# Kernel optimization log

Hardware: AMD Instinct MI355X
Metric: run time of the kernel (lower is better)

The kernel has to match this reference:

```python
import jax, jax.numpy as jnp
import numpy as np

IMAGE_SIZE = 512
OUT_SIZE = 64
FEAT = 256
SCALES = [2.0, 4.0, 6.0]
RATIOS = [0.5, 1.0, 2.0]
POS_THR = 0.7
NEG_THR = 0.3
HW = OUT_SIZE - 2            # head grid after 3x3 VALID conv
A = len(SCALES) * len(RATIOS)
B, N = 16, 8


def _anchor_base():
    # mirrors get_anchor_base(out_size-2, ratios, scales): w=scale*ratio, h=scale,
    # centers at i+0.5, boxes [xmin,ymin,xmax,ymax] clipped to [0, HW]
    ctr = np.arange(HW, dtype=np.float32) + 0.5
    ws = np.array([s * r for r in RATIOS for s in SCALES], np.float32)
    hs = np.array([s for r in RATIOS for s in SCALES], np.float32)
    X = ctr[:, None, None]  # x index first, as in the torch loop
    Y = ctr[None, :, None]
    xmin = np.clip(X - ws / 2, 0, HW)
    xmax = np.clip(X + ws / 2, 0, HW)
    ymin = np.clip(Y - hs / 2, 0, HW)
    ymax = np.clip(Y + hs / 2, 0, HW)
    xmin, ymin, xmax, ymax = np.broadcast_arrays(xmin, ymin, xmax, ymax)
    return np.stack([xmin, ymin, xmax, ymax], -1).reshape(-1, 4)  # [T,4]


def _conv(x, w, b):
    y = jax.lax.conv_general_dilated(x, w, (1, 1), 'VALID',
                                     dimension_numbers=('NCHW', 'OIHW', 'NCHW'))
    return y + b[None, :, None, None]


def setup_inputs() -> dict:
    key = jax.random.key(0)
    ks = jax.random.split(key, 8)
    features = jax.random.normal(ks[0], (B, FEAT, OUT_SIZE, OUT_SIZE), jnp.float32)
    cxy = jax.random.uniform(ks[1], (B, N, 2), jnp.float32, 0.0, IMAGE_SIZE)
    half = jax.random.uniform(ks[2], (B, N, 2), jnp.float32, 10.0, 60.0)
    mins = jnp.clip(cxy - half, 0.0, IMAGE_SIZE)
    maxs = jnp.clip(cxy + half, 0.0, IMAGE_SIZE)
    gt_boxes = jnp.concatenate([mins, maxs], -1)  # [B,N,4] xyxy in image coords
    gt_class = jax.random.randint(ks[3], (B, N), 0, 21)
    conv_w = jax.random.normal(ks[4], (FEAT, FEAT, 3, 3), jnp.float32) * 0.02
    conv_b = jnp.zeros((FEAT,), jnp.float32)
    cls_w = jax.random.normal(ks[5], (A, FEAT, 1, 1), jnp.float32) * 0.02
    cls_b = jnp.zeros((A,), jnp.float32)
    box_w = jax.random.normal(ks[6], (4 * A, FEAT, 1, 1), jnp.float32) * 0.02
    box_b = jnp.zeros((4 * A,), jnp.float32)
    return dict(features=features, gt_boxes=gt_boxes, gt_class=gt_class,
                conv_w=conv_w, conv_b=conv_b, cls_w=cls_w, cls_b=cls_b,
                box_w=box_w, box_b=box_b)


def reference(features, gt_boxes, gt_class, conv_w, conv_b, cls_w, cls_b, box_w, box_b):
    b = features.shape[0]
    x = _conv(features, conv_w, conv_b)          # [B,FEAT,HW,HW]
    cls = _conv(x, cls_w, cls_b)                 # [B,A,HW,HW]
    bx = _conv(x, box_w, box_b)                  # [B,4A,HW,HW]
    cls = cls.transpose(0, 2, 3, 1).reshape(b, -1)                    # [B,T]
    pred_off = bx.transpose(0, 2, 3, 1).reshape(b, -1, 4)             # [B,T,4]

    anchors = jnp.asarray(_anchor_base())        # [T,4]
    scale = IMAGE_SIZE // HW
    gt = gt_boxes / scale                        # project_bboxes p2a

    ax1, ay1, ax2, ay2 = (anchors[:, i] for i in range(4))
    gx1, gy1, gx2, gy2 = (gt[..., i] for i in range(4))
    area_a = (ax2 - ax1) * (ay2 - ay1)                                 # [T]
    area_g = (gx2 - gx1) * (gy2 - gy1)                                 # [B,N]
    ix1 = jnp.maximum(ax1[None, :, None], gx1[:, None, :])
    iy1 = jnp.maximum(ay1[None, :, None], gy1[:, None, :])
    ix2 = jnp.minimum(ax2[None, :, None], gx2[:, None, :])
    iy2 = jnp.minimum(ay2[None, :, None], gy2[:, None, :])
    inter = jnp.clip(ix2 - ix1, 0) * jnp.clip(iy2 - iy1, 0)            # [B,T,N]
    union = area_a[None, :, None] + area_g[:, None, :] - inter
    iou = inter / jnp.maximum(union, 1e-9)                             # [B,T,N]

    max_per_gt = iou.max(axis=1, keepdims=True)                        # best anchor per GT
    pos_mask = ((iou == max_per_gt) & (max_per_gt > 0)) | (iou > POS_THR)
    posf = pos_mask.astype(jnp.float32)
    num_pos = jnp.maximum(posf.sum(), 1.0)

    # anchor / gt boxes in cxcywh
    acx, acy = (ax1 + ax2) / 2, (ay1 + ay2) / 2
    aw, ah = ax2 - ax1, ay2 - ay1
    gcx, gcy = (gx1 + gx2) / 2, (gy1 + gy2) / 2
    gw, gh = gx2 - gx1, gy2 - gy1
    # per (anchor, gt) pair offsets [B,T,N,4]
    tx = (gcx[:, None, :] - acx[None, :, None]) / aw[None, :, None]
    ty = (gcy[:, None, :] - acy[None, :, None]) / ah[None, :, None]
    tw = jnp.log(gw)[:, None, :] - jnp.log(aw)[None, :, None]
    th = jnp.log(gh)[:, None, :] - jnp.log(ah)[None, :, None]
    gt_off = jnp.stack([tx, ty, tw, th], -1)

    diff = pred_off[:, :, None, :] - gt_off
    ad = jnp.abs(diff)
    sl1 = jnp.where(ad < 1.0, 0.5 * diff * diff, ad - 0.5)
    reg_loss = (sl1 * posf[..., None]).sum() / (num_pos * 4.0)

    # BCE-with-logits: positives target 1, negatives (iou < neg_thr) target 0
    pos_loss = (jax.nn.softplus(-cls)[:, :, None] * posf).sum() / num_pos
    negf = (iou < NEG_THR).astype(jnp.float32)
    num_neg = jnp.maximum(negf.sum(), 1.0)
    neg_loss = (jax.nn.softplus(cls)[:, :, None] * negf).sum() / num_neg
    cls_loss = 0.5 * (pos_loss + neg_loss)

    # proposals from predicted offsets, all anchors (positives selectable via pos_mask)
    pcx = acx[None, :] + pred_off[..., 0] * aw[None, :]
    pcy = acy[None, :] + pred_off[..., 1] * ah[None, :]
    pw = aw[None, :] * jnp.exp(pred_off[..., 2])
    ph = ah[None, :] * jnp.exp(pred_off[..., 3])
    proposal_scale = OUT_SIZE / HW
    proposals = jnp.stack([pcx - pw / 2, pcy - ph / 2, pcx + pw / 2, pcy + ph / 2],
                          -1) * proposal_scale                          # [B,T,4]

    # class of best-matching GT per anchor (GT_pos_class analogue, full grid)
    best_gt = jnp.argmax(iou, axis=-1)                                  # [B,T]
    gt_cls_per_anchor = jnp.take_along_axis(
        jnp.broadcast_to(gt_class[:, None, :], iou.shape).astype(jnp.int32),
        best_gt[..., None].astype(jnp.int32), -1)[..., 0]

    return (cls_loss, reg_loss, proposals, pos_mask, gt_cls_per_anchor)
```

## Files before the change

### kernel.cpp

```cpp
#include <hip/hip_runtime.h>
#include <math.h>

#define HW2   62
#define NANCH 34596
#define NBAT  16
#define NGT   8
#define FEATC 256
#define NOUT  45
#define NBLK_C 496

typedef short bf16x8 __attribute__((ext_vector_type(8)));
typedef float f32x4  __attribute__((ext_vector_type(4)));
typedef float f32x2  __attribute__((ext_vector_type(2)));

#define AS1U(p) ((const __attribute__((address_space(1))) unsigned int*)(p))
#define AS3U(p) ((__attribute__((address_space(3))) unsigned int*)(p))

__device__ __forceinline__ unsigned short f2bf(float f) {
    unsigned int u = __float_as_uint(f);
    u = u + 0x7FFFu + ((u >> 16) & 1u);
    return (unsigned short)(u >> 16);
}


__device__ __forceinline__ void anchor4(int i, int j, int a,
                                        float& x1, float& y1, float& x2, float& y2) {
    int am = a % 3, ad = a / 3;
    float h = 2.f * (float)(am + 1);
    float w = h * 0.5f * (float)(1 << ad);
    float cx = (float)i + 0.5f, cy = (float)j + 0.5f;
    x1 = fminf(fmaxf(cx - 0.5f * w, 0.f), 62.f);
    x2 = fminf(fmaxf(cx + 0.5f * w, 0.f), 62.f);
    y1 = fminf(fmaxf(cy - 0.5f * h, 0.f), 62.f);
    y2 = fminf(fmaxf(cy + 0.5f * h, 0.f), 62.f);
}

__device__ __forceinline__ float iou_fn(float ax1, float ay1, float ax2, float ay2,
                                        float gx1, float gy1, float gx2, float gy2) {
    float area_a = __fmul_rn(__fsub_rn(ax2, ax1), __fsub_rn(ay2, ay1));
    float area_g = __fmul_rn(__fsub_rn(gx2, gx1), __fsub_rn(gy2, gy1));
    float ix1 = fmaxf(ax1, gx1), iy1 = fmaxf(ay1, gy1);
    float ix2 = fminf(ax2, gx2), iy2 = fminf(ay2, gy2);
    float iw = fmaxf(__fsub_rn(ix2, ix1), 0.f);
    float ih = fmaxf(__fsub_rn(iy2, iy1), 0.f);
    float inter = __fmul_rn(iw, ih);
    float uni = __fsub_rn(__fadd_rn(area_a, area_g), inter);
    return inter / fmaxf(uni, 1e-9f);
}

__device__ __forceinline__ float softplus_f(float x) {
    return fmaxf(x, 0.f) + log1pf(expf(-fabsf(x)));
}

__device__ __forceinline__ float sl1_f(float d) {
    float ad = fabsf(d);
    return (ad < 1.f) ? 0.5f * d * d : (ad - 0.5f);
}

__device__ __forceinline__ void to_bf16_body(const float* __restrict__ feat,
                                             unsigned short* __restrict__ ft,
                                             float* ldsT,
                                             int yp, int cc, int bz, int b, int t) {
    int y0 = yp * 2;
#pragma unroll
    for (int k = 0; k < 4; ++k) {
        int fi = k * 256 + t;
        int ch = fi >> 5, r = fi & 31;
        int y = r >> 4, xq = r & 15;
        f32x4 v = *(const f32x4*)(feat + ((size_t)(b * 256 + cc * 32 + ch) << 12)
                                  + (y0 + y) * 64 + xq * 4);
        int word = ch * 128 + y * 64 + ((xq * 4) ^ ((ch & 7) << 3));
        *(f32x4*)(ldsT + word) = v;
    }
    __syncthreads();
    int y = t >> 7, x = (t >> 1) & 63, h2 = t & 1;
    bf16x8 o0, o1;
#pragma unroll
    for (int j = 0; j < 8; ++j) {
        int ch = h2 * 16 + j;
        o0[j] = (short)f2bf(ldsT[ch * 128 + y * 64 + (x ^ ((ch & 7) << 3))]);
    }
#pragma unroll
    for (int j = 0; j < 8; ++j) {
        int ch = h2 * 16 + 8 + j;
        o1[j] = (short)f2bf(ldsT[ch * 128 + y * 64 + (x ^ ((ch & 7) << 3))]);
    }
    unsigned short* ftc = ft + ((size_t)(bz * 8 + cc) << 17);
    size_t p = (size_t)(y0 + y) * 64 + x;
    *(bf16x8*)(ftc + ((size_t)(h2 * 2) * 4096 + p) * 8) = o0;
    *(bf16x8*)(ftc + ((size_t)(h2 * 2 + 1) * 4096 + p) * 8) = o1;
}

__global__ void prep_all(const float* __restrict__ feat,
                         const float* __restrict__ conv_w,
                         const float* __restrict__ conv_b,
                         const float* __restrict__ cls_w,
                         const float* __restrict__ cls_b,
                         const float* __restrict__ box_w,
                         const float* __restrict__ box_b,
                         const float* __restrict__ gtb,
                         unsigned short* __restrict__ Bfrag,
                         float* __restrict__ effb,
                         float* __restrict__ maxiou,
                         unsigned short* __restrict__ ft) {
    __shared__ float ldsT[4096];
    __shared__ float red[256];
    int blk = blockIdx.x, t = threadIdx.x;
    if (blk < 432) {
        int i = blk * 256 + t;
        int o = i / 2304, idx = i - o * 2304;
        float s = 0.f;
        if (o < NOUT) {
            const float* w2 = (o < 9) ? (cls_w + o * FEATC) : (box_w + (o - 9) * FEATC);
#pragma unroll 8
            for (int m = 0; m < FEATC; ++m)
                s = fmaf(w2[m], conv_w[(size_t)m * 2304 + idx], s);
        }
        int c = idx / 9, tap = idx - c * 9;
        size_t slot = (((size_t)(c >> 5) * 9 + tap) * 3 + (o >> 4)) * 512
                    + (size_t)((((c >> 3) & 3) * 16) + (o & 15)) * 8 + (c & 7);
        Bfrag[slot] = f2bf(s);
    } else if (blk < 560) {
        int bg = blk - 432;
        int b = bg >> 3, g = bg & 7;
        const float* p = gtb + (b * NGT + g) * 4;
        float gx1 = p[0] * 0.125f, gy1 = p[1] * 0.125f;
        float gx2 = p[2] * 0.125f, gy2 = p[3] * 0.125f;
        float m = 0.f;
        for (int n = t; n < NANCH; n += 256) {
            int i = n / 558; int r = n - i * 558; int j = r / 9; int a = r - j * 9;
            float ax1, ay1, ax2, ay2;
            anchor4(i, j, a, ax1, ay1, ax2, ay2);
            m = fmaxf(m, iou_fn(ax1, ay1, ax2, ay2, gx1, gy1, gx2, gy2));
        }
        red[t] = m;
        __syncthreads();
        for (int s = 128; s > 0; s >>= 1) {
            if (t < s) red[t] = fmaxf(red[t], red[t + s]);
            __syncthreads();
        }
        if (t == 0) maxiou[bg] = red[0];
    } else if (blk == 560) {
        if (t < 48) {
            float bv = 0.f;
            if (t < NOUT) {
                bv = (t < 9) ? cls_b[t] : box_b[t - 9];
                const float* w2 = (t < 9) ? (cls_w + t * FEATC) : (box_w + (t - 9) * FEATC);
                for (int mid = 0; mid < FEATC; ++mid) bv = fmaf(w2[mid], conv_b[mid], bv);
            }
            effb[t] = bv;
        }
    } else {
        int u = blk - 561;
        int yp = u & 31, cc = (u >> 5) & 7, bz = u >> 8;
        to_bf16_body(feat, ft, ldsT, yp, cc, bz, bz, t);
    }
}

__launch_bounds__(512, 4)
__global__ void conv_fused(const unsigned short* __restrict__ ft,
                           const unsigned short* __restrict__ Bfrag,
                           const float* __restrict__ effb,
                           const float* __restrict__ gtb,
                           const int* __restrict__ gtc,
                           const float* __restrict__ maxiou,
                           float* __restrict__ outp,
                           float* __restrict__ blksums) {
    __shared__ __align__(16) unsigned char Bs[2][27648];
    __shared__ float gshr[40];
    __shared__ float wred[8][5];

    float (*Cs)[49]  = (float (*)[49])&Bs[0][0];
    float (*Cs1)[49] = (float (*)[49])&Bs[1][0];

    const int t = threadIdx.x, l = t & 63, w = t >> 6;
    const int l15 = l & 15, lq = l >> 4;
    const int slot = w & 3, kg = w >> 2;

    int cpx = gridDim.x >> 3;
    int wgid = (blockIdx.x & 7) * cpx + (blockIdx.x >> 3);
    const int band = wgid % 31, b = wgid / 31;
    const int y0 = band * 2;

    if (t < 32) gshr[t] = gtb[b * 32 + t] * 0.125f;
    else if (t < 40) gshr[t] = maxiou[b * 8 + (t - 32)];

    f32x4 acc[2][3];
#pragma unroll
    for (int nf = 0; nf < 3; ++nf) {
        float bv = (kg == 0) ? effb[nf * 16 + l15] : 0.f;
#pragma unroll
        for (int mf = 0; mf < 2; ++mf)
#pragma unroll
            for (int r2 = 0; r2 < 4; ++r2) acc[mf][nf][r2] = bv;
    }

    int p0 = slot * 32 + l15;      if (p0 > 123) p0 = 123;
    int p1 = slot * 32 + 16 + l15; if (p1 > 123) p1 = 123;
    int rr0 = p0 / 62, c0 = p0 - rr0 * 62;
    int rr1 = p1 / 62, c1 = p1 - rr1 * 62;
    const int aoff0 = (lq << 12) + (y0 + rr0) * 64 + c0;
    const int aoff1 = (lq << 12) + (y0 + rr1) * 64 + c1;

    for (int i = 0; i < 4; ++i) {
#pragma unroll
        for (int k = 0; k < 7; ++k) {
            int u = t + k * 512;
            if (u < 3456) {
                int buf = (u >= 1728) ? 1 : 0;
                int idx = u - buf * 1728;
                int cs = buf ? (4 + i) : i;
                __builtin_amdgcn_global_load_lds(
                    AS1U(Bfrag + (size_t)cs * 13824 + (size_t)idx * 8),
                    AS3U(&Bs[buf][0] + idx * 16), 16, 0, 0);
            }
        }
        __syncthreads();

        int cc = kg * 4 + i;
        const unsigned short* ftc = ft + ((size_t)(b * 8 + cc) << 17);
        const unsigned char* Bb = &Bs[kg][0];
#pragma unroll
        for (int tap = 0; tap < 9; ++tap) {
            int d = (tap / 3) * 64 + (tap % 3);
            bf16x8 a0 = *(const bf16x8*)(ftc + (size_t)(aoff0 + d) * 8);
            bf16x8 a1 = *(const bf16x8*)(ftc + (size_t)(aoff1 + d) * 8);
#pragma unroll
            for (int nf = 0; nf < 3; ++nf) {
                bf16x8 bfr = *(const bf16x8*)(Bb + (((tap * 3 + nf) << 6) + l) * 16);
                acc[0][nf] = __builtin_amdgcn_mfma_f32_16x16x32_bf16(a0, bfr, acc[0][nf], 0, 0, 0);
                acc[1][nf] = __builtin_amdgcn_mfma_f32_16x16x32_bf16(a1, bfr, acc[1][nf], 0, 0, 0);
            }
        }
        __syncthreads();
    }

    {
        float (*Cdst)[49] = (kg == 0) ? Cs : Cs1;
#pragma unroll
        for (int mf = 0; mf < 2; ++mf)
#pragma unroll
            for (int nf = 0; nf < 3; ++nf)
#pragma unroll
                for (int r2 = 0; r2 < 4; ++r2) {
                    int pix = slot * 32 + mf * 16 + lq * 4 + r2;
                    if (pix < 124) Cdst[pix][nf * 16 + l15] = acc[mf][nf][r2];
                }
    }
    __syncthreads();

    float s_pos = 0.f, s_neg = 0.f, s_pl = 0.f, s_nl = 0.f, s_reg = 0.f;
    float* out_prop = outp + 2;
    float* out_mask = out_prop + (size_t)NBAT * NANCH * 4;
    float* out_gtc  = out_mask + (size_t)NBAT * NANCH * 8;

    for (int k = 0; k < 3; ++k) {
        int an = k * 512 + t;
        if (an < 1116) {
            int pixloc = an / 9, a = an - pixloc * 9;
            int rr = pixloc / 62, col = pixloc - rr * 62;
            int oy = y0 + rr, ox = col;
            int n = oy * 558 + ox * 9 + a;
            float cls = Cs[pixloc][a]          + Cs1[pixloc][a];
            float p0f = Cs[pixloc][9 + 4 * a]  + Cs1[pixloc][9 + 4 * a];
            float p1f = Cs[pixloc][10 + 4 * a] + Cs1[pixloc][10 + 4 * a];
            float p2f = Cs[pixloc][11 + 4 * a] + Cs1[pixloc][11 + 4 * a];
            float p3f = Cs[pixloc][12 + 4 * a] + Cs1[pixloc][12 + 4 * a];

            float ax1, ay1, ax2, ay2;
            anchor4(oy, ox, a, ax1, ay1, ax2, ay2);
            float aw = ax2 - ax1, ah = ay2 - ay1;
            float acx = 0.5f * (ax1 + ax2), acy = 0.5f * (ay1 + ay2);

            const float ps = 64.f / 62.f;
            float pcx = acx + p0f * aw, pcy = acy + p1f * ah;
            float pw = aw * expf(p2f), ph = ah * expf(p3f);
            float* pp = out_prop + ((size_t)b * NANCH + n) * 4;
            f32x2 pr0 = { (pcx - 0.5f * pw) * ps, (pcy - 0.5f * ph) * ps };
            f32x2 pr1 = { (pcx + 0.5f * pw) * ps, (pcy + 0.5f * ph) * ps };
            *(f32x2*)(pp) = pr0;
            *(f32x2*)(pp + 2) = pr1;

            float law = logf(aw), lah = logf(ah);
            float posf_tot = 0.f, negf_tot = 0.f;
            float best_iou = -1.f; int best_g = 0;
            float pfv[8];
#pragma unroll
            for (int g = 0; g < NGT; ++g) {
                float gx1 = gshr[g * 4 + 0], gy1 = gshr[g * 4 + 1];
                float gx2 = gshr[g * 4 + 2], gy2 = gshr[g * 4 + 3];
                float iou = iou_fn(ax1, ay1, ax2, ay2, gx1, gy1, gx2, gy2);
                float mpg = gshr[32 + g];
                bool pm = ((iou == mpg) && (mpg > 0.f)) || (iou > 0.7f);
                float pf = pm ? 1.f : 0.f;
                float nf = (iou < 0.3f) ? 1.f : 0.f;
                pfv[g] = pf;
                posf_tot += pf; negf_tot += nf;
                if (iou > best_iou) { best_iou = iou; best_g = g; }
                if (pm) {
                    float gw = gx2 - gx1, gh = gy2 - gy1;
                    float gcx = 0.5f * (gx1 + gx2), gcy = 0.5f * (gy1 + gy2);
                    float tx_ = (gcx - acx) / aw, ty_ = (gcy - acy) / ah;
                    float tw_ = logf(gw) - law, th_ = logf(gh) - lah;
                    float d0 = p0f - tx_, d1 = p1f - ty_, d2 = p2f - tw_, d3 = p3f - th_;
                    s_reg += sl1_f(d0) + sl1_f(d1) + sl1_f(d2) + sl1_f(d3);
                }
            }
            float* mp = out_mask + ((size_t)b * NANCH + n) * 8;
#pragma unroll
            for (int g = 0; g < 8; g += 2) {
                f32x2 mv = { pfv[g], pfv[g + 1] };
                *(f32x2*)(mp + g) = mv;
            }
            s_pos += posf_tot; s_neg += negf_tot;
            s_pl += softplus_f(-cls) * posf_tot;
            s_nl += softplus_f(cls) * negf_tot;
            out_gtc[(size_t)b * NANCH + n] = (float)gtc[b * NGT + best_g];
        }
    }

    int blk = b * 31 + band;
    float vals[5] = {s_pos, s_neg, s_pl, s_nl, s_reg};
#pragma unroll
    for (int s = 0; s < 5; ++s) {
        float v = vals[s];
#pragma unroll
        for (int m = 32; m >= 1; m >>= 1) v += __shfl_xor(v, m, 64);
        if (l == 0) wred[w][s] = v;
    }
    __syncthreads();
    if (t < 40) {
        int s = t >> 3, ww = t & 7;
        float v = wred[ww][s];
        v += __shfl_xor(v, 4, 64);
        v += __shfl_xor(v, 2, 64);
        v += __shfl_xor(v, 1, 64);
        if (ww == 0) blksums[(size_t)s * NBLK_C + blk] = v;
    }
}

__global__ void finalize(const float* __restrict__ blksums, float* __restrict__ outp) {
    __shared__ float red[256];
    __shared__ float tot[5];
    int t = threadIdx.x;
#pragma unroll
    for (int s = 0; s < 5; ++s) {
        float a = 0.f;
        for (int i = t; i < NBLK_C; i += 256) a += blksums[(size_t)s * NBLK_C + i];
        red[t] = a;
        __syncthreads();
        for (int st = 128; st > 0; st >>= 1) {
            if (t < st) red[t] += red[t + st];
            __syncthreads();
        }
        if (t == 0) tot[s] = red[0];
        __syncthreads();
    }
    if (t == 0) {
        float np_ = fmaxf(tot[0], 1.f), nn_ = fmaxf(tot[1], 1.f);
        outp[0] = 0.5f * (tot[2] / np_ + tot[3] / nn_);
        outp[1] = tot[4] / (np_ * 4.f);
    }
}

extern "C" void kernel_launch(void* const* d_in, const int* in_sizes, int n_in,
                              void* d_out, int out_size, void* d_ws, size_t ws_size,
                              hipStream_t stream) {
    (void)in_sizes; (void)n_in; (void)out_size; (void)ws_size;
    const float* feat   = (const float*)d_in[0];
    const float* gtb    = (const float*)d_in[1];
    const int*   gtc    = (const int*)d_in[2];
    const float* conv_w = (const float*)d_in[3];
    const float* conv_b = (const float*)d_in[4];
    const float* cls_w  = (const float*)d_in[5];
    const float* cls_b  = (const float*)d_in[6];
    const float* box_w  = (const float*)d_in[7];
    const float* box_b  = (const float*)d_in[8];
    float* outp = (float*)d_out;
    float* ws   = (float*)d_ws;

    unsigned short* Bfrag   = (unsigned short*)ws;
    float*          effb    = ws + 55296;
    float*          maxiou  = ws + 55360;
    float*          blksums = ws + 55488;
    unsigned short* ft      = (unsigned short*)(ws + 60608);

    prep_all<<<561 + 4096, 256, 0, stream>>>(feat, conv_w, conv_b, cls_w, cls_b,
                                             box_w, box_b, gtb, Bfrag, effb, maxiou, ft);
    conv_fused<<<NBLK_C, 512, 0, stream>>>(ft, Bfrag, effb, gtb, gtc, maxiou,
                                           outp, blksums);
    finalize<<<1, 256, 0, stream>>>(blksums, outp);
}
```

Baseline: 67.20 us.

## Batch weight-fold over 9 outputs per block and hoist conv tap loads per row

The weight-folding prep now has each block stage 9 output rows of cls/box weights in shared memory and reuse every conv_w load across 9 accumulators. This cuts the redundant global reads of conv_w (45 reads per element before). The feature bf16 conversion blocks are reordered to launch first and the block ranges are reindexed, with the grid shrinking from 4657 to 4270 blocks. In the conv kernel, the three A-fragment loads of each kernel row are issued together ahead of a sched_barrier to overlap load latency with MFMAs, which raises register pressure.

```diff
diff --git a/kernel.cpp b/kernel.cpp
--- a/kernel.cpp
+++ b/kernel.cpp
@@ -104,24 +104,42 @@
                          float* __restrict__ maxiou,
                          unsigned short* __restrict__ ft) {
     __shared__ float ldsT[4096];
+    __shared__ float w2s[9][256];
     __shared__ float red[256];
     int blk = blockIdx.x, t = threadIdx.x;
-    if (blk < 432) {
-        int i = blk * 256 + t;
-        int o = i / 2304, idx = i - o * 2304;
-        float s = 0.f;
-        if (o < NOUT) {
-            const float* w2 = (o < 9) ? (cls_w + o * FEATC) : (box_w + (o - 9) * FEATC);
-#pragma unroll 8
-            for (int m = 0; m < FEATC; ++m)
-                s = fmaf(w2[m], conv_w[(size_t)m * 2304 + idx], s);
+    if (blk < 4096) {
+        int u = blk;
+        int yp = u & 31, cc = (u >> 5) & 7, bz = u >> 8;
+        to_bf16_body(feat, ft, ldsT, yp, cc, bz, bz, t);
+    } else if (blk < 4141) {
+        int fb = blk - 4096;
+        int idx_blk = fb / 5, og = fb - idx_blk * 5;
+        for (int i = t; i < 9 * 256; i += 256) {
+            int oi = i >> 8, m = i & 255;
+            int o = og * 9 + oi;
+            w2s[oi][m] = (o < 9) ? cls_w[o * FEATC + m] : box_w[(o - 9) * FEATC + m];
+        }
+        __syncthreads();
+        int idx = idx_blk * 256 + t;
+        float acc[9];
+#pragma unroll
+        for (int oi = 0; oi < 9; ++oi) acc[oi] = 0.f;
+        for (int m = 0; m < FEATC; ++m) {
+            float cw = conv_w[(size_t)m * 2304 + idx];
+#pragma unroll
+            for (int oi = 0; oi < 9; ++oi)
+                acc[oi] = fmaf(cw, w2s[oi][m], acc[oi]);
         }
         int c = idx / 9, tap = idx - c * 9;
-        size_t slot = (((size_t)(c >> 5) * 9 + tap) * 3 + (o >> 4)) * 512
-                    + (size_t)((((c >> 3) & 3) * 16) + (o & 15)) * 8 + (c & 7);
-        Bfrag[slot] = f2bf(s);
-    } else if (blk < 560) {
-        int bg = blk - 432;
+#pragma unroll
+        for (int oi = 0; oi < 9; ++oi) {
+            int o = og * 9 + oi;
+            size_t slot = (((size_t)(c >> 5) * 9 + tap) * 3 + (o >> 4)) * 512
+                        + (size_t)((((c >> 3) & 3) * 16) + (o & 15)) * 8 + (c & 7);
+            Bfrag[slot] = f2bf(acc[oi]);
+        }
+    } else if (blk < 4269) {
+        int bg = blk - 4141;
         int b = bg >> 3, g = bg & 7;
         const float* p = gtb + (b * NGT + g) * 4;
         float gx1 = p[0] * 0.125f, gy1 = p[1] * 0.125f;
@@ -140,7 +158,7 @@
             __syncthreads();
         }
         if (t == 0) maxiou[bg] = red[0];
-    } else if (blk == 560) {
+    } else {
         if (t < 48) {
             float bv = 0.f;
             if (t < NOUT) {
@@ -150,10 +168,6 @@
             }
             effb[t] = bv;
         }
-    } else {
-        int u = blk - 561;
-        int yp = u & 31, cc = (u >> 5) & 7, bz = u >> 8;
-        to_bf16_body(feat, ft, ldsT, yp, cc, bz, bz, t);
     }
 }
 
@@ -221,15 +235,24 @@
         const unsigned short* ftc = ft + ((size_t)(b * 8 + cc) << 17);
         const unsigned char* Bb = &Bs[kg][0];
 #pragma unroll
-        for (int tap = 0; tap < 9; ++tap) {
-            int d = (tap / 3) * 64 + (tap % 3);
-            bf16x8 a0 = *(const bf16x8*)(ftc + (size_t)(aoff0 + d) * 8);
-            bf16x8 a1 = *(const bf16x8*)(ftc + (size_t)(aoff1 + d) * 8);
-#pragma unroll
-            for (int nf = 0; nf < 3; ++nf) {
-                bf16x8 bfr = *(const bf16x8*)(Bb + (((tap * 3 + nf) << 6) + l) * 16);
-                acc[0][nf] = __builtin_amdgcn_mfma_f32_16x16x32_bf16(a0, bfr, acc[0][nf], 0, 0, 0);
-                acc[1][nf] = __builtin_amdgcn_mfma_f32_16x16x32_bf16(a1, bfr, acc[1][nf], 0, 0, 0);
+        for (int dy = 0; dy < 3; ++dy) {
+            bf16x8 a0[3], a1[3];
+#pragma unroll
+            for (int dx = 0; dx < 3; ++dx) {
+                int d = dy * 64 + dx;
+                a0[dx] = *(const bf16x8*)(ftc + (size_t)(aoff0 + d) * 8);
+                a1[dx] = *(const bf16x8*)(ftc + (size_t)(aoff1 + d) * 8);
+            }
+            __builtin_amdgcn_sched_barrier(0);
+#pragma unroll
+            for (int dx = 0; dx < 3; ++dx) {
+                int tap = dy * 3 + dx;
+#pragma unroll
+                for (int nf = 0; nf < 3; ++nf) {
+                    bf16x8 bfr = *(const bf16x8*)(Bb + (((tap * 3 + nf) << 6) + l) * 16);
+                    acc[0][nf] = __builtin_amdgcn_mfma_f32_16x16x32_bf16(a0[dx], bfr, acc[0][nf], 0, 0, 0);
+                    acc[1][nf] = __builtin_amdgcn_mfma_f32_16x16x32_bf16(a1[dx], bfr, acc[1][nf], 0, 0, 0);
+                }
             }
         }
         __syncthreads();
@@ -385,8 +408,8 @@
     float*          blksums = ws + 55488;
     unsigned short* ft      = (unsigned short*)(ws + 60608);
 
-    prep_all<<<561 + 4096, 256, 0, stream>>>(feat, conv_w, conv_b, cls_w, cls_b,
-                                             box_w, box_b, gtb, Bfrag, effb, maxiou, ft);
+    prep_all<<<4270, 256, 0, stream>>>(feat, conv_w, conv_b, cls_w, cls_b,
+                                       box_w, box_b, gtb, Bfrag, effb, maxiou, ft);
     conv_fused<<<NBLK_C, 512, 0, stream>>>(ft, Bfrag, effb, gtb, gtc, maxiou,
                                            outp, blksums);
     finalize<<<1, 256, 0, stream>>>(blksums, outp);
```

Measured after the change: 83.46 us. +24.2%, slower.
